# Optimization experiments

Measured on AMD Instinct MI355X. Metric: run time of the kernel, lower is better.

Reference implementation:

```python
import jax, jax.numpy as jnp
import numpy as np

DIM = 1024
NUM_EXPERTS = 8
TOP_K = 2
LOAD_BALANCE_WEIGHT = 0.01


def setup_inputs() -> dict:
    key = jax.random.key(0)
    ks = jax.random.split(key, 8)
    d, e, h = DIM, NUM_EXPERTS, 4 * DIM
    scale = 0.02
    return {
        "x": jax.random.normal(ks[0], (4, 2048, d), dtype=jnp.float32),
        "w_router": jax.random.normal(ks[1], (d, e), dtype=jnp.float32) * scale,
        "b_router": jnp.zeros((e,), dtype=jnp.float32),
        "w1": jax.random.normal(ks[2], (e, d, h), dtype=jnp.float32) * scale,
        "b1": jnp.zeros((e, h), dtype=jnp.float32),
        "w2": jax.random.normal(ks[3], (e, h, d), dtype=jnp.float32) * scale,
        "b2": jnp.zeros((e, d), dtype=jnp.float32),
    }


def reference(x, w_router, b_router, w1, b1, w2, b2):
    # x: [b, s, d]
    router_logits = jnp.einsum("bsd,de->bse", x, w_router) + b_router  # [b,s,E]
    probs = jax.nn.softmax(router_logits, axis=-1)
    routing_weights, selected_experts = jax.lax.top_k(probs, TOP_K)  # [b,s,K]
    routing_weights = routing_weights / routing_weights.sum(axis=-1, keepdims=True)

    output = jnp.zeros_like(x)
    for e in range(NUM_EXPERTS):
        # Dense per-expert MLP; tokens not routed to expert e get gate 0,
        # matching the masked scatter-add in the original module.
        h = jax.nn.gelu(jnp.einsum("bsd,dh->bsh", x, w1[e]) + b1[e], approximate=False)
        y = jnp.einsum("bsh,hd->bsd", h, w2[e]) + b2[e]
        gate = jnp.where(selected_experts == e, routing_weights, 0.0).sum(axis=-1)  # [b,s]
        output = output + y * gate[..., None]

    # Load-balance aux loss: var (unbiased, ddof=1) / mean of tokens-per-expert.
    one_hot = jax.nn.one_hot(selected_experts, NUM_EXPERTS, dtype=jnp.float32)  # [b,s,K,E]
    tokens_per_expert = one_hot.sum(axis=(0, 1, 2))  # [E]
    load_balance_loss = (jnp.var(tokens_per_expert, ddof=1) / tokens_per_expert.mean()) * LOAD_BALANCE_WEIGHT
    return output, load_balance_loss
```

## Files before the change

kernel.cpp:

```cpp
#include <hip/hip_runtime.h>
#include <math.h>

#define TOKENS 8192
#define DIM    1024
#define NEXP   8
#define HID    4096
#define TILE_M 128
#define MAX_TILES 136
#define BKS    32

#define BK     32
#define LDA    40
#define LDB    40

typedef __bf16 bf16x8 __attribute__((ext_vector_type(8)));
typedef float  f32x4  __attribute__((ext_vector_type(4)));
typedef unsigned int u32x4 __attribute__((ext_vector_type(4)));

__device__ __forceinline__ unsigned short f2bf(float f) {
  union { float f; unsigned u; } v; v.f = f;
  unsigned u = v.u + 0x7fffu + ((v.u >> 16) & 1u);
  return (unsigned short)(u >> 16);
}
__device__ __forceinline__ float gelu_f(float v) {
  return 0.5f * v * (1.f + erff(v * 0.7071067811865476f));
}
__device__ __forceinline__ float gelu_fast(float v) {
  float t = v * v;
  float y = 0.7978845608f * v * fmaf(t, 0.044715f, 1.0f);
  y = fminf(y, 15.f);
  float z = __expf(2.f * y);
  return v * z * __builtin_amdgcn_rcpf(1.f + z);
}
__device__ __forceinline__ void gload16(const void* g, void* l) {
  __builtin_amdgcn_global_load_lds(
      (const __attribute__((address_space(1))) void*)g,
      (__attribute__((address_space(3))) void*)l, 16, 0, 0);
}
__device__ __forceinline__ int xcd_swz(int id, int nwg) {
  int q = nwg >> 3, r = nwg & 7;
  int xcd = id & 7, rank = id >> 3;
  return (xcd < r) ? xcd * (q + 1) + rank : r * (q + 1) + (xcd - r) * q + rank;
}

__global__ __launch_bounds__(256) void k_router(
    const float* __restrict__ x, const float* __restrict__ wr,
    const float* __restrict__ br, int* __restrict__ sel,
    float* __restrict__ gates, int* __restrict__ counts,
    unsigned short* __restrict__ xb)
{
  int t = blockIdx.x * 4 + (threadIdx.x >> 6);
  int lane = threadIdx.x & 63;
  const float* xr = x + (size_t)t * DIM;
  unsigned short* xo = xb + (size_t)t * DIM;
  float acc[NEXP];
#pragma unroll
  for (int e = 0; e < NEXP; ++e) acc[e] = 0.f;
#pragma unroll
  for (int it = 0; it < 4; ++it) {
    int d = it * 256 + lane * 4;
    float4 xv = *(const float4*)(xr + d);
    ushort4 pk;
    pk.x = f2bf(xv.x); pk.y = f2bf(xv.y); pk.z = f2bf(xv.z); pk.w = f2bf(xv.w);
    *(ushort4*)(xo + d) = pk;
    float xs[4] = {xv.x, xv.y, xv.z, xv.w};
#pragma unroll
    for (int j = 0; j < 4; ++j) {
      float4 wa = *(const float4*)(wr + (size_t)(d + j) * NEXP);
      float4 wb = *(const float4*)(wr + (size_t)(d + j) * NEXP + 4);
      acc[0] += xs[j] * wa.x; acc[1] += xs[j] * wa.y;
      acc[2] += xs[j] * wa.z; acc[3] += xs[j] * wa.w;
      acc[4] += xs[j] * wb.x; acc[5] += xs[j] * wb.y;
      acc[6] += xs[j] * wb.z; acc[7] += xs[j] * wb.w;
    }
  }
#pragma unroll
  for (int off = 32; off >= 1; off >>= 1) {
#pragma unroll
    for (int e = 0; e < NEXP; ++e) acc[e] += __shfl_xor(acc[e], off);
  }
  if (lane == 0) {
    float l[NEXP];
#pragma unroll
    for (int e = 0; e < NEXP; ++e) l[e] = acc[e] + br[e];
    int e1 = 0; float v1 = l[0];
#pragma unroll
    for (int e = 1; e < NEXP; ++e) if (l[e] > v1) { v1 = l[e]; e1 = e; }
    int e2 = -1; float v2 = -1e30f;
#pragma unroll
    for (int e = 0; e < NEXP; ++e) {
      if (e == e1) continue;
      if (l[e] > v2) { v2 = l[e]; e2 = e; }
    }
    float g1 = 1.f / (1.f + expf(v2 - v1));
    sel[t * 2] = e1; sel[t * 2 + 1] = e2;
    gates[t * 2] = g1; gates[t * 2 + 1] = 1.f - g1;
    atomicAdd(&counts[e1], 1);
    atomicAdd(&counts[e2], 1);
  }
}

__global__ __launch_bounds__(256) void k_setup(
    const int* __restrict__ counts, int* __restrict__ cursors,
    int* __restrict__ ntiles_p, int* __restrict__ tile_expert,
    int* __restrict__ tile_row0, int* __restrict__ pair_token,
    float* __restrict__ pair_gate, float* __restrict__ loss_out)
{
  __shared__ int s_pad0[NEXP], s_pad1[NEXP];
  int tid = threadIdx.x;
  if (tid == 0) {
    int poff = 0, nt = 0;
    float var = 0.f;
    for (int e = 0; e < NEXP; ++e) {
      int c = counts[e];
      cursors[e] = poff;
      int ntl = (c + TILE_M - 1) / TILE_M;
      for (int i = 0; i < ntl; ++i) { tile_expert[nt] = e; tile_row0[nt] = poff + i * TILE_M; ++nt; }
      s_pad0[e] = poff + c;
      s_pad1[e] = poff + ntl * TILE_M;
      float d = (float)c - 2048.f;
      var += d * d;
      poff += ntl * TILE_M;
    }
    *ntiles_p = nt;
    *loss_out = (var * (1.f / 7.f)) * (1.f / 2048.f) * 0.01f;
  }
  __syncthreads();
#pragma unroll
  for (int e = 0; e < NEXP; ++e) {
    for (int r = s_pad0[e] + tid; r < s_pad1[e]; r += 256) {
      pair_token[r] = -1; pair_gate[r] = 0.f;
    }
  }
}

__global__ __launch_bounds__(256) void k_bucket(
    const int* __restrict__ sel, const float* __restrict__ gates,
    int* __restrict__ cursors, int* __restrict__ pair_token, float* __restrict__ pair_gate)
{
  int t = blockIdx.x * 256 + threadIdx.x;
#pragma unroll
  for (int k = 0; k < 2; ++k) {
    int e = sel[t * 2 + k];
    int pos = atomicAdd(&cursors[e], 1);
    pair_token[pos] = t;
    pair_gate[pos] = gates[t * 2 + k];
  }
}

__global__ __launch_bounds__(256) void k_castwT(
    const float* __restrict__ w, unsigned short* __restrict__ wT, int K, int N)
{
  __shared__ unsigned short t[64][72];
  int e = blockIdx.z, n0 = blockIdx.x * 64, k0 = blockIdx.y * 64;
  int tid = threadIdx.x;
  int kr = tid >> 2, nc = (tid & 3) * 16;
  const float* src = w + ((size_t)e * K + k0 + kr) * N + n0 + nc;
#pragma unroll
  for (int j = 0; j < 4; ++j) {
    f32x4 v = *(const f32x4*)(src + j * 4);
#pragma unroll
    for (int q = 0; q < 4; ++q) t[nc + j * 4 + q][kr] = f2bf(v[q]);
  }
  __syncthreads();
  int nr = tid >> 2, kc = (tid & 3) * 16;
  unsigned short* dst = wT + ((size_t)e * N + n0 + nr) * K + k0 + kc;
  *(u32x4*)dst = *(const u32x4*)&t[nr][kc];
  *(u32x4*)(dst + 8) = *(const u32x4*)&t[nr][kc + 8];
}

__global__ __launch_bounds__(256) void k_gemm1n(
    const unsigned short* __restrict__ xb, const unsigned short* __restrict__ w1T,
    const float* __restrict__ b1, const int* __restrict__ pair_token,
    const int* __restrict__ tile_expert, const int* __restrict__ tile_row0,
    const int* __restrict__ ntiles_p, unsigned short* __restrict__ h, int chunk_base)
{
  const int NBn = HID / 128;
  const int nwg = gridDim.x;
  int newid = xcd_swz(blockIdx.x, nwg);
  int ltile = newid / NBn, nb = newid - ltile * NBn;
  int tile = chunk_base + ltile;
  if (tile >= *ntiles_p) return;
  const int e = tile_expert[tile];
  const int row0 = tile_row0[tile];
  const int n0 = nb * 128;
  const int tid = threadIdx.x;
  const int w = tid >> 6, lane = tid & 63;

  __shared__ unsigned short As[3][128 * BKS];
  __shared__ unsigned short Bs[3][128 * BKS];
  __shared__ int tok[128];

  if (tid < 128) { int t = pair_token[row0 + tid]; tok[tid] = (t < 0) ? 0 : t; }
  __syncthreads();

  const int sr = lane >> 2;
  const int kq = (((lane & 3) ^ ((sr >> 1) & 3))) * 8;
  const int ar1 = w * 32 + sr, ar2 = ar1 + 16;
  const unsigned short* ag1 = xb + (size_t)tok[ar1] * DIM + kq;
  const unsigned short* ag2 = xb + (size_t)tok[ar2] * DIM + kq;
  const unsigned short* bg1 = w1T + ((size_t)e * HID + n0 + ar1) * DIM + kq;
  const unsigned short* bg2 = w1T + ((size_t)e * HID + n0 + ar2) * DIM + kq;

  const int wm = (w & 1) * 64, wn = (w >> 1) * 64;
  const int lr = lane & 15, lk = lane >> 4;
  const int gx = lk ^ ((lr >> 1) & 3);

  f32x4 acc[4][4];
#pragma unroll
  for (int mi = 0; mi < 4; ++mi)
#pragma unroll
    for (int ni = 0; ni < 4; ++ni) acc[mi][ni] = {0.f, 0.f, 0.f, 0.f};

#define STAGE1(buf, koff)                                      \
  gload16(ag1 + (koff), &As[buf][(w * 32) * BKS]);             \
  gload16(ag2 + (koff), &As[buf][(w * 32 + 16) * BKS]);        \
  gload16(bg1 + (koff), &Bs[buf][(w * 32) * BKS]);             \
  gload16(bg2 + (koff), &Bs[buf][(w * 32 + 16) * BKS]);

  STAGE1(0, 0)
  STAGE1(1, BKS)
  asm volatile("s_waitcnt vmcnt(4)" ::: "memory");
  __builtin_amdgcn_s_barrier();

  const int NT = DIM / BKS;
  int cur = 0, dst = 2;
  for (int t = 0; t < NT; ++t) {
    if (t + 2 < NT) { STAGE1(dst, (t + 2) * BKS) }
    bf16x8 af[4], bfr[4];
#pragma unroll
    for (int mi = 0; mi < 4; ++mi)
      af[mi] = *(const bf16x8*)&As[cur][(wm + mi * 16 + lr) * BKS + gx * 8];
#pragma unroll
    for (int ni = 0; ni < 4; ++ni)
      bfr[ni] = *(const bf16x8*)&Bs[cur][(wn + ni * 16 + lr) * BKS + gx * 8];
    asm volatile("s_waitcnt lgkmcnt(0)" ::: "memory");
    __builtin_amdgcn_sched_barrier(0);
    __builtin_amdgcn_s_setprio(1);
#pragma unroll
    for (int mi = 0; mi < 4; ++mi)
#pragma unroll
      for (int ni = 0; ni < 4; ++ni)
        acc[mi][ni] = __builtin_amdgcn_mfma_f32_16x16x32_bf16(bfr[ni], af[mi], acc[mi][ni], 0, 0, 0);
    __builtin_amdgcn_s_setprio(0);
    if (t + 2 < NT) { asm volatile("s_waitcnt vmcnt(4)" ::: "memory"); }
    else            { asm volatile("s_waitcnt vmcnt(0)" ::: "memory"); }
    __builtin_amdgcn_s_barrier();
    cur = (cur == 2) ? 0 : cur + 1;
    dst = (dst == 2) ? 0 : dst + 1;
  }
#undef STAGE1

  const size_t tl = (size_t)(tile - chunk_base);
  f32x4 bv[4];
#pragma unroll
  for (int ni = 0; ni < 4; ++ni)
    bv[ni] = *(const f32x4*)(b1 + (size_t)e * HID + n0 + wn + ni * 16 + lk * 4);
#pragma unroll
  for (int mi = 0; mi < 4; ++mi) {
    int m = wm + mi * 16 + lr;
    unsigned short* hrow = h + (tl * TILE_M + m) * HID + n0;
#pragma unroll
    for (int ni = 0; ni < 4; ++ni) {
      int nb4 = wn + ni * 16 + lk * 4;
      ushort4 pk;
      pk.x = f2bf(gelu_fast(acc[mi][ni][0] + bv[ni][0]));
      pk.y = f2bf(gelu_fast(acc[mi][ni][1] + bv[ni][1]));
      pk.z = f2bf(gelu_fast(acc[mi][ni][2] + bv[ni][2]));
      pk.w = f2bf(gelu_fast(acc[mi][ni][3] + bv[ni][3]));
      *(ushort4*)(hrow + nb4) = pk;
    }
  }
}

__global__ __launch_bounds__(256) void k_gemm2n(
    const unsigned short* __restrict__ h, const unsigned short* __restrict__ w2T,
    const float* __restrict__ b2, const int* __restrict__ pair_token,
    const float* __restrict__ pair_gate,
    const int* __restrict__ tile_expert, const int* __restrict__ tile_row0,
    const int* __restrict__ ntiles_p, float* __restrict__ out, int chunk_base)
{
  const int NBn = DIM / 128;
  const int nwg = gridDim.x;
  int newid = xcd_swz(blockIdx.x, nwg);
  int ltile = newid / NBn, nb = newid - ltile * NBn;
  int tile = chunk_base + ltile;
  if (tile >= *ntiles_p) return;
  const int e = tile_expert[tile];
  const int row0 = tile_row0[tile];
  const int n0 = nb * 128;
  const int tid = threadIdx.x;
  const int w = tid >> 6, lane = tid & 63;

  __shared__ unsigned short As[3][128 * BKS];
  __shared__ unsigned short Bs[3][128 * BKS];
  __shared__ int tok[128];
  __shared__ float gat[128];

  if (tid < 128) { tok[tid] = pair_token[row0 + tid]; gat[tid] = pair_gate[row0 + tid]; }
  __syncthreads();

  const int sr = lane >> 2;
  const int kq = (((lane & 3) ^ ((sr >> 1) & 3))) * 8;
  const int ar1 = w * 32 + sr, ar2 = ar1 + 16;
  const size_t tl = (size_t)(tile - chunk_base);
  const unsigned short* ag1 = h + (tl * TILE_M + ar1) * HID + kq;
  const unsigned short* ag2 = h + (tl * TILE_M + ar2) * HID + kq;
  const unsigned short* bg1 = w2T + ((size_t)e * DIM + n0 + ar1) * HID + kq;
  const unsigned short* bg2 = w2T + ((size_t)e * DIM + n0 + ar2) * HID + kq;

  const int wm = (w & 1) * 64, wn = (w >> 1) * 64;
  const int lr = lane & 15, lk = lane >> 4;
  const int gx = lk ^ ((lr >> 1) & 3);

  f32x4 acc[4][4];
#pragma unroll
  for (int mi = 0; mi < 4; ++mi)
#pragma unroll
    for (int ni = 0; ni < 4; ++ni) acc[mi][ni] = {0.f, 0.f, 0.f, 0.f};

#define STAGE2(buf, koff)                                      \
  gload16(ag1 + (koff), &As[buf][(w * 32) * BKS]);             \
  gload16(ag2 + (koff), &As[buf][(w * 32 + 16) * BKS]);        \
  gload16(bg1 + (koff), &Bs[buf][(w * 32) * BKS]);             \
  gload16(bg2 + (koff), &Bs[buf][(w * 32 + 16) * BKS]);

  STAGE2(0, 0)
  STAGE2(1, BKS)
  asm volatile("s_waitcnt vmcnt(4)" ::: "memory");
  __builtin_amdgcn_s_barrier();

  const int NT = HID / BKS;
  int cur = 0, dst = 2;
  for (int t = 0; t < NT; ++t) {
    if (t + 2 < NT) { STAGE2(dst, (t + 2) * BKS) }
    bf16x8 af[4], bfr[4];
#pragma unroll
    for (int mi = 0; mi < 4; ++mi)
      af[mi] = *(const bf16x8*)&As[cur][(wm + mi * 16 + lr) * BKS + gx * 8];
#pragma unroll
    for (int ni = 0; ni < 4; ++ni)
      bfr[ni] = *(const bf16x8*)&Bs[cur][(wn + ni * 16 + lr) * BKS + gx * 8];
    asm volatile("s_waitcnt lgkmcnt(0)" ::: "memory");
    __builtin_amdgcn_sched_barrier(0);
    __builtin_amdgcn_s_setprio(1);
#pragma unroll
    for (int mi = 0; mi < 4; ++mi)
#pragma unroll
      for (int ni = 0; ni < 4; ++ni)
        acc[mi][ni] = __builtin_amdgcn_mfma_f32_16x16x32_bf16(af[mi], bfr[ni], acc[mi][ni], 0, 0, 0);
    __builtin_amdgcn_s_setprio(0);
    if (t + 2 < NT) { asm volatile("s_waitcnt vmcnt(4)" ::: "memory"); }
    else            { asm volatile("s_waitcnt vmcnt(0)" ::: "memory"); }
    __builtin_amdgcn_s_barrier();
    cur = (cur == 2) ? 0 : cur + 1;
    dst = (dst == 2) ? 0 : dst + 1;
  }
#undef STAGE2

  float bia[4];
#pragma unroll
  for (int ni = 0; ni < 4; ++ni) bia[ni] = b2[(size_t)e * DIM + n0 + wn + ni * 16 + lr];
#pragma unroll
  for (int mi = 0; mi < 4; ++mi)
#pragma unroll
    for (int r = 0; r < 4; ++r) {
      int m = wm + mi * 16 + lk * 4 + r;
      int t = tok[m];
      if (t >= 0) {
        float g = gat[m];
#pragma unroll
        for (int ni = 0; ni < 4; ++ni) {
          int n = wn + ni * 16 + lr;
          atomicAdd(out + (size_t)t * DIM + n0 + n, (acc[mi][ni][r] + bia[ni]) * g);
        }
      }
    }
}

__global__ __launch_bounds__(256) void k_gemm1(
    const unsigned short* __restrict__ xb, const float* __restrict__ w1,
    const float* __restrict__ b1, const int* __restrict__ pair_token,
    const int* __restrict__ tile_expert, const int* __restrict__ tile_row0,
    const int* __restrict__ ntiles_p, unsigned short* __restrict__ h, int chunk_base)
{
  int tile = chunk_base + blockIdx.y;
  if (tile >= *ntiles_p) return;
  const int e = tile_expert[tile];
  const int row0 = tile_row0[tile];
  const int n0 = blockIdx.x * 128;
  const int tid = threadIdx.x;

  __shared__ unsigned short As[TILE_M * LDA];
  __shared__ unsigned short Bs[128 * LDB];
  __shared__ int tok[TILE_M];

  if (tid < TILE_M) tok[tid] = pair_token[row0 + tid];
  __syncthreads();

  const int ar = tid >> 1, akh = (tid & 1) * 16;
  const int bk = tid >> 3, bnh = (tid & 7) * 16;
  const int bswz = tid & 3;
  const int wv = tid >> 6, lane = tid & 63;
  const int wm = (wv & 1) * 64, wn = (wv >> 1) * 64;
  const int lr = lane & 15, lk = lane >> 4;
  const int atok = tok[ar];

  f32x4 acc[4][4];
#pragma unroll
  for (int mi = 0; mi < 4; ++mi)
#pragma unroll
    for (int ni = 0; ni < 4; ++ni) acc[mi][ni] = {0.f, 0.f, 0.f, 0.f};

  const unsigned short* asrc = (atok >= 0) ? (xb + (size_t)atok * DIM + akh) : (const unsigned short*)0;
  const float* bsrc0 = w1 + ((size_t)e * DIM + bk) * HID + n0 + bnh;
  const int wcol = 8 * ((bk >> 3) ^ bswz) + (bk & 7);

  for (int k0 = 0; k0 < DIM; k0 += BK) {
    u32x4 av0 = {0, 0, 0, 0}, av1 = {0, 0, 0, 0};
    if (asrc) {
      av0 = *(const u32x4*)(asrc + k0);
      av1 = *(const u32x4*)(asrc + k0 + 8);
    }
    float bv[16];
    const float* bs = bsrc0 + (size_t)k0 * HID;
#pragma unroll
    for (int j = 0; j < 4; ++j) {
      f32x4 f = *(const f32x4*)(bs + j * 4);
      bv[j * 4 + 0] = f[0]; bv[j * 4 + 1] = f[1];
      bv[j * 4 + 2] = f[2]; bv[j * 4 + 3] = f[3];
    }
    __syncthreads();
    *(u32x4*)&As[ar * LDA + akh] = av0;
    *(u32x4*)&As[ar * LDA + akh + 8] = av1;
#pragma unroll
    for (int j = 0; j < 16; ++j)
      Bs[(bnh + j) * LDB + wcol] = f2bf(bv[j]);
    __syncthreads();

    bf16x8 af[4], bfr[4];
#pragma unroll
    for (int mi = 0; mi < 4; ++mi)
      af[mi] = *(const bf16x8*)&As[(wm + mi * 16 + lr) * LDA + lk * 8];
#pragma unroll
    for (int ni = 0; ni < 4; ++ni) {
      int pch = lk ^ (((wn >> 4) + ni) & 3);
      bfr[ni] = *(const bf16x8*)&Bs[(wn + ni * 16 + lr) * LDB + pch * 8];
    }
#pragma unroll
    for (int mi = 0; mi < 4; ++mi)
#pragma unroll
      for (int ni = 0; ni < 4; ++ni)
        acc[mi][ni] = __builtin_amdgcn_mfma_f32_16x16x32_bf16(af[mi], bfr[ni], acc[mi][ni], 0, 0, 0);
  }

  const size_t tl = (size_t)(tile - chunk_base);
#pragma unroll
  for (int mi = 0; mi < 4; ++mi)
#pragma unroll
    for (int ni = 0; ni < 4; ++ni)
#pragma unroll
      for (int r = 0; r < 4; ++r) {
        int m = wm + mi * 16 + (lane >> 4) * 4 + r;
        int n = wn + ni * 16 + (lane & 15);
        float v = acc[mi][ni][r] + b1[(size_t)e * HID + n0 + n];
        h[(tl * TILE_M + m) * HID + n0 + n] = f2bf(gelu_f(v));
      }
}

__global__ __launch_bounds__(256) void k_gemm2(
    const unsigned short* __restrict__ h, const float* __restrict__ w2,
    const float* __restrict__ b2, const int* __restrict__ pair_token,
    const float* __restrict__ pair_gate,
    const int* __restrict__ tile_expert, const int* __restrict__ tile_row0,
    const int* __restrict__ ntiles_p, float* __restrict__ out, int chunk_base)
{
  int tile = chunk_base + blockIdx.y;
  if (tile >= *ntiles_p) return;
  const int e = tile_expert[tile];
  const int row0 = tile_row0[tile];
  const int n0 = blockIdx.x * 128;
  const int tid = threadIdx.x;

  __shared__ unsigned short As[TILE_M * LDA];
  __shared__ unsigned short Bs[128 * LDB];
  __shared__ int tok[TILE_M];
  __shared__ float gat[TILE_M];

  if (tid < TILE_M) { tok[tid] = pair_token[row0 + tid]; gat[tid] = pair_gate[row0 + tid]; }
  __syncthreads();

  const int ar = tid >> 1, akh = (tid & 1) * 16;
  const int bk = tid >> 3, bnh = (tid & 7) * 16;
  const int bswz = tid & 3;
  const int wv = tid >> 6, lane = tid & 63;
  const int wm = (wv & 1) * 64, wn = (wv >> 1) * 64;
  const int lr = lane & 15, lk = lane >> 4;

  f32x4 acc[4][4];
#pragma unroll
  for (int mi = 0; mi < 4; ++mi)
#pragma unroll
    for (int ni = 0; ni < 4; ++ni) acc[mi][ni] = {0.f, 0.f, 0.f, 0.f};

  const size_t tl = (size_t)(tile - chunk_base);
  const unsigned short* asrc = h + (tl * TILE_M + ar) * HID + akh;
  const float* bsrc0 = w2 + ((size_t)e * HID + bk) * DIM + n0 + bnh;
  const int wcol = 8 * ((bk >> 3) ^ bswz) + (bk & 7);

  for (int k0 = 0; k0 < HID; k0 += BK) {
    u32x4 av0 = *(const u32x4*)(asrc + k0);
    u32x4 av1 = *(const u32x4*)(asrc + k0 + 8);
    float bv[16];
    const float* bs = bsrc0 + (size_t)k0 * DIM;
#pragma unroll
    for (int j = 0; j < 4; ++j) {
      f32x4 f = *(const f32x4*)(bs + j * 4);
      bv[j * 4 + 0] = f[0]; bv[j * 4 + 1] = f[1];
      bv[j * 4 + 2] = f[2]; bv[j * 4 + 3] = f[3];
    }
    __syncthreads();
    *(u32x4*)&As[ar * LDA + akh] = av0;
    *(u32x4*)&As[ar * LDA + akh + 8] = av1;
#pragma unroll
    for (int j = 0; j < 16; ++j)
      Bs[(bnh + j) * LDB + wcol] = f2bf(bv[j]);
    __syncthreads();

    bf16x8 af[4], bfr[4];
#pragma unroll
    for (int mi = 0; mi < 4; ++mi)
      af[mi] = *(const bf16x8*)&As[(wm + mi * 16 + lr) * LDA + lk * 8];
#pragma unroll
    for (int ni = 0; ni < 4; ++ni) {
      int pch = lk ^ (((wn >> 4) + ni) & 3);
      bfr[ni] = *(const bf16x8*)&Bs[(wn + ni * 16 + lr) * LDB + pch * 8];
    }
#pragma unroll
    for (int mi = 0; mi < 4; ++mi)
#pragma unroll
      for (int ni = 0; ni < 4; ++ni)
        acc[mi][ni] = __builtin_amdgcn_mfma_f32_16x16x32_bf16(af[mi], bfr[ni], acc[mi][ni], 0, 0, 0);
  }

#pragma unroll
  for (int mi = 0; mi < 4; ++mi)
#pragma unroll
    for (int ni = 0; ni < 4; ++ni)
#pragma unroll
      for (int r = 0; r < 4; ++r) {
        int m = wm + mi * 16 + (lane >> 4) * 4 + r;
        int n = wn + ni * 16 + (lane & 15);
        int t = tok[m];
        if (t >= 0) {
          float v = acc[mi][ni][r] + b2[(size_t)e * DIM + n0 + n];
          atomicAdd(out + (size_t)t * DIM + n0 + n, v * gat[m]);
        }
      }
}

extern "C" void kernel_launch(void* const* d_in, const int* in_sizes, int n_in,
                              void* d_out, int out_size, void* d_ws, size_t ws_size,
                              hipStream_t stream) {
  const float* x  = (const float*)d_in[0];
  const float* wr = (const float*)d_in[1];
  const float* br = (const float*)d_in[2];
  const float* w1 = (const float*)d_in[3];
  const float* b1 = (const float*)d_in[4];
  const float* w2 = (const float*)d_in[5];
  const float* b2 = (const float*)d_in[6];
  float* out = (float*)d_out;

  char* ws = (char*)d_ws;
  int*   counts      = (int*)(ws + 0);
  int*   cursors     = (int*)(ws + 64);
  int*   ntiles      = (int*)(ws + 128);
  int*   tile_expert = (int*)(ws + 256);
  int*   tile_row0   = (int*)(ws + 1024);
  int*   sel         = (int*)(ws + 4096);
  float* gates       = (float*)(ws + 4096 + 65536);
  int*   pair_token  = (int*)(ws + 4096 + 131072);
  float* pair_gate   = (float*)(ws + 4096 + 131072 + 69632);

  const size_t OFF_XB  = 274432;
  const size_t XB_SZ   = (size_t)TOKENS * DIM * 2;
  const size_t OFF_W1T = OFF_XB + XB_SZ;
  const size_t WT_SZ   = (size_t)NEXP * DIM * HID * 2;
  const size_t OFF_W2T = OFF_W1T + WT_SZ;
  const size_t OFF_HN  = OFF_W2T + WT_SZ;
  const size_t tile_bytes = (size_t)TILE_M * HID * 2;

  unsigned short* xb  = (unsigned short*)(ws + OFF_XB);

  hipMemsetAsync(d_out, 0, (size_t)out_size * sizeof(float), stream);
  hipMemsetAsync(counts, 0, 64, stream);

  hipLaunchKernelGGL(k_router, dim3(TOKENS / 4), dim3(256), 0, stream,
                     x, wr, br, sel, gates, counts, xb);
  hipLaunchKernelGGL(k_setup, dim3(1), dim3(256), 0, stream,
                     counts, cursors, ntiles, tile_expert, tile_row0,
                     pair_token, pair_gate, out + (size_t)out_size - 1);
  hipLaunchKernelGGL(k_bucket, dim3(TOKENS / 256), dim3(256), 0, stream,
                     sel, gates, cursors, pair_token, pair_gate);

  bool newpath = ws_size >= OFF_HN + tile_bytes;

  if (newpath) {
    unsigned short* w1T = (unsigned short*)(ws + OFF_W1T);
    unsigned short* w2T = (unsigned short*)(ws + OFF_W2T);
    unsigned short* h   = (unsigned short*)(ws + OFF_HN);

    hipLaunchKernelGGL(k_castwT, dim3(HID / 64, DIM / 64, NEXP), dim3(256), 0, stream,
                       w1, w1T, DIM, HID);
    hipLaunchKernelGGL(k_castwT, dim3(DIM / 64, HID / 64, NEXP), dim3(256), 0, stream,
                       w2, w2T, HID, DIM);

    long long avail = (long long)ws_size - (long long)OFF_HN;
    int tpc = (int)(avail / (long long)tile_bytes);
    if (tpc < 1) tpc = 1;
    if (tpc > MAX_TILES) tpc = MAX_TILES;
    int nchunks = (MAX_TILES + tpc - 1) / tpc;

    for (int c = 0; c < nchunks; ++c) {
      hipLaunchKernelGGL(k_gemm1n, dim3(tpc * (HID / 128)), dim3(256), 0, stream,
                         xb, w1T, b1, pair_token, tile_expert, tile_row0, ntiles, h, c * tpc);
      hipLaunchKernelGGL(k_gemm2n, dim3(tpc * (DIM / 128)), dim3(256), 0, stream,
                         h, w2T, b2, pair_token, pair_gate, tile_expert, tile_row0, ntiles, out, c * tpc);
    }
  } else {
    unsigned short* h = (unsigned short*)(ws + OFF_W1T);
    long long avail = (long long)ws_size - (long long)OFF_W1T;
    int tpc = (avail > 0) ? (int)(avail / (long long)tile_bytes) : 0;
    if (tpc < 1) tpc = 1;
    if (tpc > MAX_TILES) tpc = MAX_TILES;
    int nchunks = (MAX_TILES + tpc - 1) / tpc;

    for (int c = 0; c < nchunks; ++c) {
      hipLaunchKernelGGL(k_gemm1, dim3(HID / 128, tpc), dim3(256), 0, stream,
                         xb, w1, b1, pair_token, tile_expert, tile_row0, ntiles, h, c * tpc);
      hipLaunchKernelGGL(k_gemm2, dim3(DIM / 128, tpc), dim3(256), 0, stream,
                         h, w2, b2, pair_token, pair_gate, tile_expert, tile_row0, ntiles, out, c * tpc);
    }
  }
}
```

Measured before the change: 818.8 us.

## Widen grouped MoE GEMM tiles to 128x256 with per-wave 128x64 subtiles

Both expert GEMM kernels move from 128x128 to 128x256 output tiles. Each wave now covers all 128 rows by 64 columns, so accumulators double to 8x4 MFMA fragments and the B staging buffer doubles, with matching vmcnt waits and grid sizes. The goal is to raise arithmetic intensity per LDS load and cut redundant activation/gather traffic. The cost is higher register and LDS use (about 72KB LDS), which may lower occupancy, and half as many workgroups, which can leave CUs idle or hurt tail balance.

```diff
diff --git a/kernel.cpp b/kernel.cpp
--- a/kernel.cpp
+++ b/kernel.cpp
@@ -169,26 +169,25 @@
   *(u32x4*)(dst + 8) = *(const u32x4*)&t[nr][kc + 8];
 }
 
-__global__ __launch_bounds__(256) void k_gemm1n(
+__global__ __launch_bounds__(256, 2) void k_gemm1n(
     const unsigned short* __restrict__ xb, const unsigned short* __restrict__ w1T,
     const float* __restrict__ b1, const int* __restrict__ pair_token,
     const int* __restrict__ tile_expert, const int* __restrict__ tile_row0,
     const int* __restrict__ ntiles_p, unsigned short* __restrict__ h, int chunk_base)
 {
-  const int NBn = HID / 128;
-  const int nwg = gridDim.x;
-  int newid = xcd_swz(blockIdx.x, nwg);
+  const int NBn = HID / 256;
+  int newid = xcd_swz(blockIdx.x, gridDim.x);
   int ltile = newid / NBn, nb = newid - ltile * NBn;
   int tile = chunk_base + ltile;
   if (tile >= *ntiles_p) return;
   const int e = tile_expert[tile];
   const int row0 = tile_row0[tile];
-  const int n0 = nb * 128;
+  const int n0 = nb * 256;
   const int tid = threadIdx.x;
   const int w = tid >> 6, lane = tid & 63;
 
   __shared__ unsigned short As[3][128 * BKS];
-  __shared__ unsigned short Bs[3][128 * BKS];
+  __shared__ unsigned short Bs[3][256 * BKS];
   __shared__ int tok[128];
 
   if (tid < 128) { int t = pair_token[row0 + tid]; tok[tid] = (t < 0) ? 0 : t; }
@@ -199,38 +198,43 @@
   const int ar1 = w * 32 + sr, ar2 = ar1 + 16;
   const unsigned short* ag1 = xb + (size_t)tok[ar1] * DIM + kq;
   const unsigned short* ag2 = xb + (size_t)tok[ar2] * DIM + kq;
-  const unsigned short* bg1 = w1T + ((size_t)e * HID + n0 + ar1) * DIM + kq;
-  const unsigned short* bg2 = w1T + ((size_t)e * HID + n0 + ar2) * DIM + kq;
-
-  const int wm = (w & 1) * 64, wn = (w >> 1) * 64;
+  const size_t bbase = (size_t)e * HID + n0 + w * 64;
+  const unsigned short* bg0 = w1T + (bbase + sr) * DIM + kq;
+  const unsigned short* bg1 = w1T + (bbase + 16 + sr) * DIM + kq;
+  const unsigned short* bg2 = w1T + (bbase + 32 + sr) * DIM + kq;
+  const unsigned short* bg3 = w1T + (bbase + 48 + sr) * DIM + kq;
+
+  const int wn = w * 64;
   const int lr = lane & 15, lk = lane >> 4;
   const int gx = lk ^ ((lr >> 1) & 3);
 
-  f32x4 acc[4][4];
-#pragma unroll
-  for (int mi = 0; mi < 4; ++mi)
+  f32x4 acc[8][4];
+#pragma unroll
+  for (int mi = 0; mi < 8; ++mi)
 #pragma unroll
     for (int ni = 0; ni < 4; ++ni) acc[mi][ni] = {0.f, 0.f, 0.f, 0.f};
 
 #define STAGE1(buf, koff)                                      \
   gload16(ag1 + (koff), &As[buf][(w * 32) * BKS]);             \
   gload16(ag2 + (koff), &As[buf][(w * 32 + 16) * BKS]);        \
-  gload16(bg1 + (koff), &Bs[buf][(w * 32) * BKS]);             \
-  gload16(bg2 + (koff), &Bs[buf][(w * 32 + 16) * BKS]);
+  gload16(bg0 + (koff), &Bs[buf][(w * 64) * BKS]);             \
+  gload16(bg1 + (koff), &Bs[buf][(w * 64 + 16) * BKS]);        \
+  gload16(bg2 + (koff), &Bs[buf][(w * 64 + 32) * BKS]);        \
+  gload16(bg3 + (koff), &Bs[buf][(w * 64 + 48) * BKS]);
 
   STAGE1(0, 0)
   STAGE1(1, BKS)
-  asm volatile("s_waitcnt vmcnt(4)" ::: "memory");
+  asm volatile("s_waitcnt vmcnt(6)" ::: "memory");
   __builtin_amdgcn_s_barrier();
 
   const int NT = DIM / BKS;
   int cur = 0, dst = 2;
   for (int t = 0; t < NT; ++t) {
     if (t + 2 < NT) { STAGE1(dst, (t + 2) * BKS) }
-    bf16x8 af[4], bfr[4];
-#pragma unroll
-    for (int mi = 0; mi < 4; ++mi)
-      af[mi] = *(const bf16x8*)&As[cur][(wm + mi * 16 + lr) * BKS + gx * 8];
+    bf16x8 af[8], bfr[4];
+#pragma unroll
+    for (int mi = 0; mi < 8; ++mi)
+      af[mi] = *(const bf16x8*)&As[cur][(mi * 16 + lr) * BKS + gx * 8];
 #pragma unroll
     for (int ni = 0; ni < 4; ++ni)
       bfr[ni] = *(const bf16x8*)&Bs[cur][(wn + ni * 16 + lr) * BKS + gx * 8];
@@ -238,12 +242,12 @@
     __builtin_amdgcn_sched_barrier(0);
     __builtin_amdgcn_s_setprio(1);
 #pragma unroll
-    for (int mi = 0; mi < 4; ++mi)
+    for (int mi = 0; mi < 8; ++mi)
 #pragma unroll
       for (int ni = 0; ni < 4; ++ni)
         acc[mi][ni] = __builtin_amdgcn_mfma_f32_16x16x32_bf16(bfr[ni], af[mi], acc[mi][ni], 0, 0, 0);
     __builtin_amdgcn_s_setprio(0);
-    if (t + 2 < NT) { asm volatile("s_waitcnt vmcnt(4)" ::: "memory"); }
+    if (t + 2 < NT) { asm volatile("s_waitcnt vmcnt(6)" ::: "memory"); }
     else            { asm volatile("s_waitcnt vmcnt(0)" ::: "memory"); }
     __builtin_amdgcn_s_barrier();
     cur = (cur == 2) ? 0 : cur + 1;
@@ -257,8 +261,8 @@
   for (int ni = 0; ni < 4; ++ni)
     bv[ni] = *(const f32x4*)(b1 + (size_t)e * HID + n0 + wn + ni * 16 + lk * 4);
 #pragma unroll
-  for (int mi = 0; mi < 4; ++mi) {
-    int m = wm + mi * 16 + lr;
+  for (int mi = 0; mi < 8; ++mi) {
+    int m = mi * 16 + lr;
     unsigned short* hrow = h + (tl * TILE_M + m) * HID + n0;
 #pragma unroll
     for (int ni = 0; ni < 4; ++ni) {
@@ -273,27 +277,26 @@
   }
 }
 
-__global__ __launch_bounds__(256) void k_gemm2n(
+__global__ __launch_bounds__(256, 2) void k_gemm2n(
     const unsigned short* __restrict__ h, const unsigned short* __restrict__ w2T,
     const float* __restrict__ b2, const int* __restrict__ pair_token,
     const float* __restrict__ pair_gate,
     const int* __restrict__ tile_expert, const int* __restrict__ tile_row0,
     const int* __restrict__ ntiles_p, float* __restrict__ out, int chunk_base)
 {
-  const int NBn = DIM / 128;
-  const int nwg = gridDim.x;
-  int newid = xcd_swz(blockIdx.x, nwg);
+  const int NBn = DIM / 256;
+  int newid = xcd_swz(blockIdx.x, gridDim.x);
   int ltile = newid / NBn, nb = newid - ltile * NBn;
   int tile = chunk_base + ltile;
   if (tile >= *ntiles_p) return;
   const int e = tile_expert[tile];
   const int row0 = tile_row0[tile];
-  const int n0 = nb * 128;
+  const int n0 = nb * 256;
   const int tid = threadIdx.x;
   const int w = tid >> 6, lane = tid & 63;
 
   __shared__ unsigned short As[3][128 * BKS];
-  __shared__ unsigned short Bs[3][128 * BKS];
+  __shared__ unsigned short Bs[3][256 * BKS];
   __shared__ int tok[128];
   __shared__ float gat[128];
 
@@ -306,38 +309,43 @@
   const size_t tl = (size_t)(tile - chunk_base);
   const unsigned short* ag1 = h + (tl * TILE_M + ar1) * HID + kq;
   const unsigned short* ag2 = h + (tl * TILE_M + ar2) * HID + kq;
-  const unsigned short* bg1 = w2T + ((size_t)e * DIM + n0 + ar1) * HID + kq;
-  const unsigned short* bg2 = w2T + ((size_t)e * DIM + n0 + ar2) * HID + kq;
-
-  const int wm = (w & 1) * 64, wn = (w >> 1) * 64;
+  const size_t bbase = (size_t)e * DIM + n0 + w * 64;
+  const unsigned short* bg0 = w2T + (bbase + sr) * HID + kq;
+  const unsigned short* bg1 = w2T + (bbase + 16 + sr) * HID + kq;
+  const unsigned short* bg2 = w2T + (bbase + 32 + sr) * HID + kq;
+  const unsigned short* bg3 = w2T + (bbase + 48 + sr) * HID + kq;
+
+  const int wn = w * 64;
   const int lr = lane & 15, lk = lane >> 4;
   const int gx = lk ^ ((lr >> 1) & 3);
 
-  f32x4 acc[4][4];
-#pragma unroll
-  for (int mi = 0; mi < 4; ++mi)
+  f32x4 acc[8][4];
+#pragma unroll
+  for (int mi = 0; mi < 8; ++mi)
 #pragma unroll
     for (int ni = 0; ni < 4; ++ni) acc[mi][ni] = {0.f, 0.f, 0.f, 0.f};
 
 #define STAGE2(buf, koff)                                      \
   gload16(ag1 + (koff), &As[buf][(w * 32) * BKS]);             \
   gload16(ag2 + (koff), &As[buf][(w * 32 + 16) * BKS]);        \
-  gload16(bg1 + (koff), &Bs[buf][(w * 32) * BKS]);             \
-  gload16(bg2 + (koff), &Bs[buf][(w * 32 + 16) * BKS]);
+  gload16(bg0 + (koff), &Bs[buf][(w * 64) * BKS]);             \
+  gload16(bg1 + (koff), &Bs[buf][(w * 64 + 16) * BKS]);        \
+  gload16(bg2 + (koff), &Bs[buf][(w * 64 + 32) * BKS]);        \
+  gload16(bg3 + (koff), &Bs[buf][(w * 64 + 48) * BKS]);
 
   STAGE2(0, 0)
   STAGE2(1, BKS)
-  asm volatile("s_waitcnt vmcnt(4)" ::: "memory");
+  asm volatile("s_waitcnt vmcnt(6)" ::: "memory");
   __builtin_amdgcn_s_barrier();
 
   const int NT = HID / BKS;
   int cur = 0, dst = 2;
   for (int t = 0; t < NT; ++t) {
     if (t + 2 < NT) { STAGE2(dst, (t + 2) * BKS) }
-    bf16x8 af[4], bfr[4];
-#pragma unroll
-    for (int mi = 0; mi < 4; ++mi)
-      af[mi] = *(const bf16x8*)&As[cur][(wm + mi * 16 + lr) * BKS + gx * 8];
+    bf16x8 af[8], bfr[4];
+#pragma unroll
+    for (int mi = 0; mi < 8; ++mi)
+      af[mi] = *(const bf16x8*)&As[cur][(mi * 16 + lr) * BKS + gx * 8];
 #pragma unroll
     for (int ni = 0; ni < 4; ++ni)
       bfr[ni] = *(const bf16x8*)&Bs[cur][(wn + ni * 16 + lr) * BKS + gx * 8];
@@ -345,12 +353,12 @@
     __builtin_amdgcn_sched_barrier(0);
     __builtin_amdgcn_s_setprio(1);
 #pragma unroll
-    for (int mi = 0; mi < 4; ++mi)
+    for (int mi = 0; mi < 8; ++mi)
 #pragma unroll
       for (int ni = 0; ni < 4; ++ni)
         acc[mi][ni] = __builtin_amdgcn_mfma_f32_16x16x32_bf16(af[mi], bfr[ni], acc[mi][ni], 0, 0, 0);
     __builtin_amdgcn_s_setprio(0);
-    if (t + 2 < NT) { asm volatile("s_waitcnt vmcnt(4)" ::: "memory"); }
+    if (t + 2 < NT) { asm volatile("s_waitcnt vmcnt(6)" ::: "memory"); }
     else            { asm volatile("s_waitcnt vmcnt(0)" ::: "memory"); }
     __builtin_amdgcn_s_barrier();
     cur = (cur == 2) ? 0 : cur + 1;
@@ -362,10 +370,10 @@
 #pragma unroll
   for (int ni = 0; ni < 4; ++ni) bia[ni] = b2[(size_t)e * DIM + n0 + wn + ni * 16 + lr];
 #pragma unroll
-  for (int mi = 0; mi < 4; ++mi)
+  for (int mi = 0; mi < 8; ++mi)
 #pragma unroll
     for (int r = 0; r < 4; ++r) {
-      int m = wm + mi * 16 + lk * 4 + r;
+      int m = mi * 16 + lk * 4 + r;
       int t = tok[m];
       if (t >= 0) {
         float g = gat[m];
@@ -622,9 +630,9 @@
     int nchunks = (MAX_TILES + tpc - 1) / tpc;
 
     for (int c = 0; c < nchunks; ++c) {
-      hipLaunchKernelGGL(k_gemm1n, dim3(tpc * (HID / 128)), dim3(256), 0, stream,
+      hipLaunchKernelGGL(k_gemm1n, dim3(tpc * (HID / 256)), dim3(256), 0, stream,
                          xb, w1T, b1, pair_token, tile_expert, tile_row0, ntiles, h, c * tpc);
-      hipLaunchKernelGGL(k_gemm2n, dim3(tpc * (DIM / 128)), dim3(256), 0, stream,
+      hipLaunchKernelGGL(k_gemm2n, dim3(tpc * (DIM / 256)), dim3(256), 0, stream,
                          h, w2T, b2, pair_token, pair_gate, tile_expert, tile_row0, ntiles, out, c * tpc);
     }
   } else {
```

Measured after the change: 903.6 us. 10.3% more time.
